# Kernel tuning notes

Measured on AMD Instinct MI355X. Metric: run time of the kernel, lower is better.

Reference implementation:

```python
import jax, jax.numpy as jnp
import numpy as np

N, E, D_IN, HD, H = 50000, 800000, 768, 64, 4
HC = HD * H


def _gat(x, src, dst, etypes, lin_w, att_src, att_dst, edge_emb, lin_edge_w, att_edge,
         bias, res_w, res_b, ln_g, ln_b):
    # Faithful PyG GATConv (edge_dim, concat=True, add_self_loops=True with
    # fill_value='mean', negative_slope=0.2) + residual + LayerNorm. Eval mode: no dropout.
    n = x.shape[0]
    h, c = att_src.shape
    xs = (x @ lin_w).reshape(n, h, c)                      # [N,H,C]
    a_src = jnp.einsum('nhc,hc->nh', xs, att_src)          # [N,H]
    a_dst = jnp.einsum('nhc,hc->nh', xs, att_dst)
    eattr = edge_emb[etypes]                               # [E,ed]
    ones = jnp.ones((etypes.shape[0],), x.dtype)
    cnt = jax.ops.segment_sum(ones, dst, num_segments=n)
    # self-loop edge_attr = mean of incoming edge attrs per node (fill_value='mean')
    loop_attr = jax.ops.segment_sum(eattr, dst, num_segments=n) / jnp.maximum(cnt, 1.0)[:, None]
    loop = jnp.arange(n, dtype=src.dtype)
    src_a = jnp.concatenate([src, loop])
    dst_a = jnp.concatenate([dst, loop])
    e_all = jnp.concatenate([eattr, loop_attr], 0)
    a_edge = jnp.einsum('ehc,hc->eh', (e_all @ lin_edge_w).reshape(-1, h, c), att_edge)
    alpha = jax.nn.leaky_relu(a_src[src_a] + a_dst[dst_a] + a_edge, 0.2)   # [Ea,H]
    # edge softmax over incoming edges of each destination node
    amax = jax.ops.segment_max(alpha, dst_a, num_segments=n)
    ea = jnp.exp(alpha - amax[dst_a])
    denom = jax.ops.segment_sum(ea, dst_a, num_segments=n)
    w = ea / (denom[dst_a] + 1e-16)
    out = jax.ops.segment_sum(xs[src_a] * w[:, :, None], dst_a, num_segments=n)
    out = out.reshape(n, h * c) + bias + (x @ res_w + res_b)
    mu = out.mean(-1, keepdims=True)
    var = jnp.mean((out - mu) ** 2, -1, keepdims=True)
    return (out - mu) * jax.lax.rsqrt(var + 1e-5) * ln_g + ln_b


def _forward(features, positions,
             fe_w1, fe_b1, fe_w2, fe_b2, fe_pos_w, fe_pos_b, fe_type_emb, fe_out_w, fe_out_b,
             g1_lin_w, g1_att_src, g1_att_dst, g1_edge_emb, g1_lin_edge_w, g1_att_edge,
             g1_bias, g1_res_w, g1_res_b, g1_ln_g, g1_ln_b,
             g2_lin_w, g2_att_src, g2_att_dst, g2_edge_emb, g2_lin_edge_w, g2_att_edge,
             g2_bias, g2_res_w, g2_res_b, g2_ln_g, g2_ln_b,
             cls_w, cls_b,
             edge_index, aspect_indices, edge_types, node_types):
    # EnhancedFeatureExtractor (eval: dropout = identity)
    hfe = jax.nn.relu(features @ fe_w1 + fe_b1) @ fe_w2 + fe_b2
    hfe = hfe + fe_type_emb[node_types] + positions[:, None] @ fe_pos_w + fe_pos_b
    hfe = hfe @ fe_out_w + fe_out_b
    src, dst = edge_index[0], edge_index[1]
    hid = _gat(hfe, src, dst, edge_types, g1_lin_w, g1_att_src, g1_att_dst, g1_edge_emb,
               g1_lin_edge_w, g1_att_edge, g1_bias, g1_res_w, g1_res_b, g1_ln_g, g1_ln_b)
    hid = jax.nn.relu(hid)
    hid = _gat(hid, src, dst, edge_types, g2_lin_w, g2_att_src, g2_att_dst, g2_edge_emb,
               g2_lin_edge_w, g2_att_edge, g2_bias, g2_res_w, g2_res_b, g2_ln_g, g2_ln_b)
    return hid[aspect_indices] @ cls_w + cls_b


def setup_inputs() -> dict:
    key = jax.random.key(0)
    ks = jax.random.split(key, 40)
    d = {}
    d['features'] = jax.random.normal(ks[0], (N, D_IN), jnp.float32)
    d['edge_index'] = jax.random.randint(ks[1], (2, E), 0, N, jnp.int32)
    d['aspect_indices'] = jax.random.randint(ks[2], (4096,), 0, N, jnp.int32)
    d['edge_types'] = jax.random.randint(ks[3], (E,), 0, 4, jnp.int32)
    d['node_types'] = jax.random.randint(ks[4], (N,), 0, 3, jnp.int32)
    d['positions'] = jax.random.uniform(ks[5], (N,), jnp.float32)

    def rn(i, shape, s=0.05):
        return s * jax.random.normal(ks[i], shape, jnp.float32)

    d['fe_w1'] = rn(6, (D_IN, HD)); d['fe_b1'] = rn(7, (HD,))
    d['fe_w2'] = rn(8, (HD, HD));   d['fe_b2'] = rn(9, (HD,))
    d['fe_pos_w'] = rn(10, (1, HD)); d['fe_pos_b'] = rn(11, (HD,))
    d['fe_type_emb'] = rn(12, (3, HD))
    d['fe_out_w'] = rn(13, (HD, HD)); d['fe_out_b'] = rn(14, (HD,))
    d['g1_lin_w'] = rn(15, (HD, HC))
    d['g1_att_src'] = rn(16, (H, HD)); d['g1_att_dst'] = rn(17, (H, HD))
    d['g1_edge_emb'] = rn(18, (4, 4)); d['g1_lin_edge_w'] = rn(19, (4, HC))
    d['g1_att_edge'] = rn(20, (H, HD))
    d['g1_bias'] = rn(21, (HC,)); d['g1_res_w'] = rn(22, (HD, HC)); d['g1_res_b'] = rn(23, (HC,))
    d['g1_ln_g'] = jnp.ones((HC,), jnp.float32); d['g1_ln_b'] = jnp.zeros((HC,), jnp.float32)
    d['g2_lin_w'] = rn(24, (HC, HD))
    d['g2_att_src'] = rn(25, (1, HD)); d['g2_att_dst'] = rn(26, (1, HD))
    d['g2_edge_emb'] = rn(27, (4, 4)); d['g2_lin_edge_w'] = rn(28, (4, HD))
    d['g2_att_edge'] = rn(29, (1, HD))
    d['g2_bias'] = rn(30, (HD,)); d['g2_res_w'] = rn(31, (HC, HD)); d['g2_res_b'] = rn(32, (HD,))
    d['g2_ln_g'] = jnp.ones((HD,), jnp.float32); d['g2_ln_b'] = jnp.zeros((HD,), jnp.float32)
    d['cls_w'] = rn(33, (HD, 3)); d['cls_b'] = rn(34, (3,))
    return d


def reference(features, edge_index, aspect_indices, edge_types, node_types, positions,
              fe_w1, fe_b1, fe_w2, fe_b2, fe_pos_w, fe_pos_b, fe_type_emb, fe_out_w, fe_out_b,
              g1_lin_w, g1_att_src, g1_att_dst, g1_edge_emb, g1_lin_edge_w, g1_att_edge,
              g1_bias, g1_res_w, g1_res_b, g1_ln_g, g1_ln_b,
              g2_lin_w, g2_att_src, g2_att_dst, g2_edge_emb, g2_lin_edge_w, g2_att_edge,
              g2_bias, g2_res_w, g2_res_b, g2_ln_g, g2_ln_b,
              cls_w, cls_b):
    return _forward(features, positions,
                    fe_w1, fe_b1, fe_w2, fe_b2, fe_pos_w, fe_pos_b, fe_type_emb, fe_out_w, fe_out_b,
                    g1_lin_w, g1_att_src, g1_att_dst, g1_edge_emb, g1_lin_edge_w, g1_att_edge,
                    g1_bias, g1_res_w, g1_res_b, g1_ln_g, g1_ln_b,
                    g2_lin_w, g2_att_src, g2_att_dst, g2_edge_emb, g2_lin_edge_w, g2_att_edge,
                    g2_bias, g2_res_w, g2_res_b, g2_ln_g, g2_ln_b,
                    cls_w, cls_b,
                    edge_index, aspect_indices, edge_types, node_types)
```

## Files before the change

### kernel.cpp

```cpp
#include <hip/hip_runtime.h>


#define LRELU(x) ((x) > 0.f ? (x) : 0.2f * (x))

typedef __attribute__((ext_vector_type(8))) short short8;
typedef __attribute__((ext_vector_type(4))) float floatx4;

__device__ __forceinline__ unsigned short f2bf(float x) {
    union { float f; unsigned int u; } v; v.f = x;
    unsigned int r = (v.u + 0x7FFFu + ((v.u >> 16) & 1u)) >> 16;
    return (unsigned short)r;
}
__device__ __forceinline__ unsigned int cvtpk(float lo, float hi) {
    unsigned int r;
    asm("v_cvt_pk_bf16_f32 %0, %1, %2" : "=v"(r) : "v"(lo), "v"(hi));
    return r;
}
__device__ __forceinline__ float bflo(unsigned int u) {
    return __uint_as_float(u << 16);
}
__device__ __forceinline__ float bfhi(unsigned int u) {
    return __uint_as_float(u & 0xFFFF0000u);
}
__device__ __forceinline__ float bf1(unsigned short u) {
    return __uint_as_float(((unsigned int)u) << 16);
}

__global__ __launch_bounds__(64) void k_tables(
    const float* __restrict__ e_emb1, const float* __restrict__ lew1,
    const float* __restrict__ ae1,
    const float* __restrict__ e_emb2, const float* __restrict__ lew2,
    const float* __restrict__ ae2,
    float* __restrict__ aet1, float* __restrict__ aet2)
{
    __shared__ float M1[16];
    __shared__ float M2[4];
    int t = threadIdx.x;
    if (t < 16) {
        int d = t >> 2, h = t & 3;
        float s = 0.f;
        for (int c = 0; c < 64; ++c) s += lew1[d * 256 + h * 64 + c] * ae1[h * 64 + c];
        M1[d * 4 + h] = s;
    }
    if (t < 4) {
        float s = 0.f;
        for (int c = 0; c < 64; ++c) s += lew2[t * 64 + c] * ae2[c];
        M2[t] = s;
    }
    __syncthreads();
    if (t < 16) {
        int ty = t >> 2, h = t & 3;
        float s = 0.f;
        for (int d = 0; d < 4; ++d) s += e_emb1[ty * 4 + d] * M1[d * 4 + h];
        aet1[ty * 4 + h] = s;
    }
    if (t < 4) {
        float s = 0.f;
        for (int d = 0; d < 4; ++d) s += e_emb2[t * 4 + d] * M2[d];
        aet2[t] = s;
    }
}

__global__ __launch_bounds__(256) void k_bswz_fe1(
    const float* __restrict__ w1, unsigned short* __restrict__ out)
{
    for (int idx = blockIdx.x * 256 + threadIdx.x; idx < 768 * 64;
         idx += gridDim.x * 256) {
        int k = idx >> 6, col = idx & 63;
        int c = k >> 6, kl = k & 63, kg = kl >> 3, j = kl & 7;
        out[((c * 8 + kg) * 64 + col) * 8 + j] = f2bf(w1[k * 64 + col]);
    }
}

template<int K, int NH>
__global__ __launch_bounds__(256) void k_bswz2(
    const float* __restrict__ B1, const float* __restrict__ B2,
    unsigned short* __restrict__ out)
{
    const int NC = 2 * NH;
    for (int idx = blockIdx.x * 256 + threadIdx.x; idx < K * NC;
         idx += gridDim.x * 256) {
        int k = idx / NC, col = idx % NC;
        float v = (col < NH) ? B1[k * NH + col] : B2[k * NH + col - NH];
        int c = k >> 6, kl = k & 63, kg = kl >> 3, j = kl & 7;
        int ct = col >> 7, cl = col & 127;
        out[(((c * (NC / 128) + ct) * 8 + kg) * 128 + cl) * 8 + j] = f2bf(v);
    }
}

__global__ __launch_bounds__(256) void k_fuse1(
    const float* __restrict__ w2, const float* __restrict__ outw,
    const float* __restrict__ b2, const float* __restrict__ posb,
    const float* __restrict__ outb, const float* __restrict__ temb,
    const float* __restrict__ posw,
    float* __restrict__ W2p, float* __restrict__ h0,
    float* __restrict__ tadd, float* __restrict__ padd)
{
    int t = threadIdx.x;
    int i = t >> 2, jq = (t & 3) * 16;
    float a16[16];
#pragma unroll
    for (int u = 0; u < 16; ++u) a16[u] = 0.f;
    for (int k = 0; k < 64; ++k) {
        float a = w2[i * 64 + k];
        const float* op = outw + k * 64 + jq;
        float4 o0 = *(const float4*)op;
        float4 o1 = *(const float4*)(op + 4);
        float4 o2 = *(const float4*)(op + 8);
        float4 o3 = *(const float4*)(op + 12);
        a16[0] += a * o0.x;  a16[1] += a * o0.y;  a16[2] += a * o0.z;  a16[3] += a * o0.w;
        a16[4] += a * o1.x;  a16[5] += a * o1.y;  a16[6] += a * o1.z;  a16[7] += a * o1.w;
        a16[8] += a * o2.x;  a16[9] += a * o2.y;  a16[10] += a * o2.z; a16[11] += a * o2.w;
        a16[12] += a * o3.x; a16[13] += a * o3.y; a16[14] += a * o3.z; a16[15] += a * o3.w;
    }
#pragma unroll
    for (int u = 0; u < 16; ++u) W2p[i * 64 + jq + u] = a16[u];
    for (int e = t; e < 320; e += 256) {
        int g = e >> 6, j = e & 63;
        float s = 0.f;
        for (int k = 0; k < 64; ++k) {
            float v;
            if (g == 0) v = b2[k] + posb[k];
            else if (g <= 3) v = temb[(g - 1) * 64 + k];
            else v = posw[k];
            s += v * outw[k * 64 + j];
        }
        if (g == 0) h0[j] = s + outb[j];
        else if (g <= 3) tadd[(g - 1) * 64 + j] = s;
        else padd[j] = s;
    }
}

__global__ __launch_bounds__(64) void k_fuse2(
    const float* __restrict__ W2p, const float* __restrict__ h0,
    const float* __restrict__ tadd, const float* __restrict__ padd,
    const float* __restrict__ lin_w, const float* __restrict__ res_w,
    const float* __restrict__ bias, const float* __restrict__ res_b,
    unsigned short* __restrict__ bz, float* __restrict__ C0,
    float* __restrict__ T, float* __restrict__ P)
{
    __shared__ float bcol[64];
    int c = blockIdx.x;
    int j = threadIdx.x;
    int cL = c & 255;
    const float* Bsrc = (c < 256) ? lin_w : res_w;
    float bv = Bsrc[j * 256 + cL];
    bcol[j] = bv;
    __syncthreads();
    float s = 0.f;
#pragma unroll 8
    for (int k = 0; k < 64; ++k) s += W2p[j * 64 + k] * bcol[k];
    int kg = j >> 3, jj = j & 7, ct = c >> 7, cl = c & 127;
    bz[((ct * 8 + kg) * 128 + cl) * 8 + jj] = f2bf(s);
    float pc = h0[j] * bv;
    float p0 = tadd[j] * bv, p1 = tadd[64 + j] * bv, p2 = tadd[128 + j] * bv;
    float pp = padd[j] * bv;
#pragma unroll
    for (int k = 32; k; k >>= 1) {
        pc += __shfl_xor(pc, k, 64); p0 += __shfl_xor(p0, k, 64);
        p1 += __shfl_xor(p1, k, 64); p2 += __shfl_xor(p2, k, 64);
        pp += __shfl_xor(pp, k, 64);
    }
    if (j == 0) {
        C0[c] = pc + ((c >= 256) ? (bias[cL] + res_b[cL]) : 0.f);
        T[c] = p0; T[512 + c] = p1; T[1024 + c] = p2;
        P[c] = pp;
    }
}

__global__ __launch_bounds__(256) void k_fe1(
    const float* __restrict__ feat, const unsigned short* __restrict__ bswz,
    const float* __restrict__ b1, unsigned short* __restrict__ t1b, int N)
{
    __shared__ __align__(16) unsigned short A_lds[8 * 64 * 8];
    int t = threadIdx.x;
    int wv = t >> 6, lane = t & 63;
    int quad = lane >> 4, l16 = lane & 15;
    long n0 = (long)blockIdx.x * 64;

    floatx4 acc[4];
#pragma unroll
    for (int i = 0; i < 4; ++i) acc[i] = (floatx4){0.f, 0.f, 0.f, 0.f};

    int srow = t >> 2, sf4 = t & 3;
    long arow = n0 + srow;
    if (arow >= N) arow = N - 1;
    const float* fbase = feat + arow * 768 + sf4 * 16;
    int col = wv * 16 + l16;

    float4 v0 = *(const float4*)(fbase);
    float4 v1 = *(const float4*)(fbase + 4);
    float4 v2 = *(const float4*)(fbase + 8);
    float4 v3 = *(const float4*)(fbase + 12);

    for (int kc = 0; kc < 768; kc += 64) {
        uint4 w0 = {cvtpk(v0.x, v0.y), cvtpk(v0.z, v0.w),
                    cvtpk(v1.x, v1.y), cvtpk(v1.z, v1.w)};
        uint4 w1p = {cvtpk(v2.x, v2.y), cvtpk(v2.z, v2.w),
                     cvtpk(v3.x, v3.y), cvtpk(v3.z, v3.w)};
        __syncthreads();
        *(uint4*)&A_lds[((2 * sf4) * 64 + srow) * 8] = w0;
        *(uint4*)&A_lds[((2 * sf4 + 1) * 64 + srow) * 8] = w1p;
        if (kc + 64 < 768) {
            v0 = *(const float4*)(fbase + kc + 64);
            v1 = *(const float4*)(fbase + kc + 68);
            v2 = *(const float4*)(fbase + kc + 72);
            v3 = *(const float4*)(fbase + kc + 76);
        }
        __syncthreads();
        int ci = kc >> 6;
#pragma unroll
        for (int s = 0; s < 2; ++s) {
            int kg0 = s * 4 + quad;
            short8 bfrag = *(const short8*)&bswz[((ci * 8 + kg0) * 64 + col) * 8];
#pragma unroll
            for (int mt = 0; mt < 4; ++mt) {
                short8 afrag = *(const short8*)&A_lds[(kg0 * 64 + mt * 16 + l16) * 8];
                acc[mt] = __builtin_amdgcn_mfma_f32_16x16x32_bf16(
                    afrag, bfrag, acc[mt], 0, 0, 0);
            }
        }
    }
    float bb = b1[col];
#pragma unroll
    for (int mt = 0; mt < 4; ++mt) {
#pragma unroll
        for (int r = 0; r < 4; ++r) {
            long m = n0 + mt * 16 + quad * 4 + r;
            if (m < N) t1b[m * 64 + col] = f2bf(fmaxf(acc[mt][r] + bb, 0.f));
        }
    }
}

template<int K, int NH, bool FADD>
__global__ __launch_bounds__(256) void k_prep(
    const unsigned short* __restrict__ A, const unsigned short* __restrict__ bswz,
    const float* __restrict__ c0_or_bias, const float* __restrict__ t_or_resb,
    const float* __restrict__ Ptab, const int* __restrict__ ntypes,
    const float* __restrict__ pos,
    unsigned short* __restrict__ xsb, float* __restrict__ resp, int N)
{
    constexpr int CT = (2 * NH) / 128;
    __shared__ __align__(16) unsigned short A_lds[8 * 64 * 8];
    int t = threadIdx.x;
    int wv = t >> 6, lane = t & 63;
    int quad = lane >> 4, l16 = lane & 15;
    long n0 = (long)blockIdx.x * 64;
    int by = blockIdx.y;

    floatx4 acc[4][2];
#pragma unroll
    for (int i = 0; i < 4; ++i)
#pragma unroll
        for (int j = 0; j < 2; ++j) acc[i][j] = (floatx4){0.f, 0.f, 0.f, 0.f};

    int srow = t >> 2, sf4 = t & 3;
    long arow = n0 + srow;
    if (arow >= N) arow = N - 1;
    const unsigned short* abase = A + arow * (long)K + sf4 * 16;

    uint4 q0 = *(const uint4*)(abase);
    uint4 q1 = *(const uint4*)(abase + 8);

    for (int kc = 0; kc < K; kc += 64) {
        __syncthreads();
        *(uint4*)&A_lds[((2 * sf4) * 64 + srow) * 8] = q0;
        *(uint4*)&A_lds[((2 * sf4 + 1) * 64 + srow) * 8] = q1;
        if (kc + 64 < K) {
            q0 = *(const uint4*)(abase + kc + 64);
            q1 = *(const uint4*)(abase + kc + 64 + 8);
        }
        __syncthreads();
        int ci = kc >> 6;
#pragma unroll
        for (int s = 0; s < 2; ++s) {
            int kg0 = s * 4 + quad;
#pragma unroll
            for (int nt = 0; nt < 2; ++nt) {
                short8 bfrag = *(const short8*)&bswz[
                    (((ci * CT + by) * 8 + kg0) * 128 + wv * 32 + nt * 16 + l16) * 8];
#pragma unroll
                for (int mt = 0; mt < 4; ++mt) {
                    short8 afrag = *(const short8*)&A_lds[(kg0 * 64 + mt * 16 + l16) * 8];
                    acc[mt][nt] = __builtin_amdgcn_mfma_f32_16x16x32_bf16(
                        afrag, bfrag, acc[mt][nt], 0, 0, 0);
                }
            }
        }
    }

    int nta[4][4];
    float posa[4][4];
    if constexpr (FADD) {
#pragma unroll
        for (int mt = 0; mt < 4; ++mt)
#pragma unroll
            for (int r = 0; r < 4; ++r) {
                long m = n0 + mt * 16 + quad * 4 + r;
                if (m < N) { nta[mt][r] = ntypes[m]; posa[mt][r] = pos[m]; }
                else       { nta[mt][r] = 0; posa[mt][r] = 0.f; }
            }
    }
#pragma unroll
    for (int nt = 0; nt < 2; ++nt) {
        int gc = by * 128 + wv * 32 + nt * 16 + l16;
        bool isl = gc < NH;
        int oc = isl ? gc : gc - NH;
        if constexpr (FADD) {
            float c0 = c0_or_bias[gc];
            float pcf = Ptab[gc];
#pragma unroll
            for (int mt = 0; mt < 4; ++mt) {
#pragma unroll
                for (int r = 0; r < 4; ++r) {
                    long m = n0 + mt * 16 + quad * 4 + r;
                    if (m < N) {
                        float val = acc[mt][nt][r] + c0 +
                                    t_or_resb[nta[mt][r] * (2 * NH) + gc] +
                                    posa[mt][r] * pcf;
                        if (isl) xsb[m * NH + oc] = f2bf(val);
                        else     resp[m * NH + oc] = val;
                    }
                }
            }
        } else {
            float badd = isl ? 0.f : (c0_or_bias[oc] + t_or_resb[oc]);
#pragma unroll
            for (int mt = 0; mt < 4; ++mt) {
#pragma unroll
                for (int r = 0; r < 4; ++r) {
                    long m = n0 + mt * 16 + quad * 4 + r;
                    if (m < N) {
                        float val = acc[mt][nt][r];
                        if (isl) xsb[m * NH + oc] = f2bf(val);
                        else     resp[m * NH + oc] = val + badd;
                    }
                }
            }
        }
    }
}

template<int H>
__global__ __launch_bounds__(256) void k_att(
    const unsigned short* __restrict__ xsb, const float* __restrict__ att_s,
    const float* __restrict__ att_d, float* __restrict__ a_src,
    float* __restrict__ a_dst, int N)
{
    int t = threadIdx.x;
    int wv = t >> 6, lane = t & 63;
    long n = (long)blockIdx.x * 4 + wv;
    if (n >= N) return;
    if (H == 4) {
        ushort4 u = *(const ushort4*)&xsb[n * 256 + lane * 4];
        float4 as = *(const float4*)&att_s[lane * 4];
        float4 ad = *(const float4*)&att_d[lane * 4];
        float x0 = bf1(u.x), x1 = bf1(u.y), x2 = bf1(u.z), x3 = bf1(u.w);
        float p = x0 * as.x + x1 * as.y + x2 * as.z + x3 * as.w;
        float q = x0 * ad.x + x1 * ad.y + x2 * ad.z + x3 * ad.w;
#pragma unroll
        for (int k = 8; k; k >>= 1) {
            p += __shfl_xor(p, k, 64);
            q += __shfl_xor(q, k, 64);
        }
        if ((lane & 15) == 0) {
            a_src[n * 4 + (lane >> 4)] = p;
            a_dst[n * 4 + (lane >> 4)] = q;
        }
    } else {
        float x = bf1(xsb[n * 64 + lane]);
        float p = x * att_s[lane];
        float q = x * att_d[lane];
#pragma unroll
        for (int k = 32; k; k >>= 1) {
            p += __shfl_xor(p, k, 64);
            q += __shfl_xor(q, k, 64);
        }
        if (lane == 0) { a_src[n] = p; a_dst[n] = q; }
    }
}

__global__ __launch_bounds__(256) void k_count(
    const int* __restrict__ dst, const int* __restrict__ et,
    int* __restrict__ cnt_t, int E)
{
    int e = blockIdx.x * 256 + threadIdx.x;
    if (e < E) atomicAdd(&cnt_t[dst[e] * 4 + et[e]], 1);
}

__global__ __launch_bounds__(256) void k_scan1(
    const int* __restrict__ cnt_t, int* __restrict__ row_off,
    int* __restrict__ blk_sums, int N)
{
    __shared__ int s[256];
    int t = threadIdx.x;
    int i = blockIdx.x * 256 + t;
    int v = 0;
    if (i < N) v = cnt_t[4 * i] + cnt_t[4 * i + 1] + cnt_t[4 * i + 2] + cnt_t[4 * i + 3];
    s[t] = v;
    __syncthreads();
    for (int off = 1; off < 256; off <<= 1) {
        int x = 0;
        if (t >= off) x = s[t - off];
        __syncthreads();
        s[t] += x;
        __syncthreads();
    }
    if (i < N) row_off[i] = s[t] - v;
    if (t == 255) blk_sums[blockIdx.x] = s[255];
}

__global__ __launch_bounds__(256) void k_scan2(int* __restrict__ blk_sums, int nb)
{
    __shared__ int s[256];
    int t = threadIdx.x;
    int v = (t < nb) ? blk_sums[t] : 0;
    s[t] = v;
    __syncthreads();
    for (int off = 1; off < 256; off <<= 1) {
        int x = 0;
        if (t >= off) x = s[t - off];
        __syncthreads();
        s[t] += x;
        __syncthreads();
    }
    if (t < nb) blk_sums[t] = s[t] - v;
}

__global__ __launch_bounds__(256) void k_scan3(
    int* __restrict__ row_off, int* __restrict__ cursor,
    const int* __restrict__ blk_sums, int N, int E)
{
    int t = threadIdx.x;
    int i = blockIdx.x * 256 + t;
    if (i < N) {
        int o = row_off[i] + blk_sums[blockIdx.x];
        row_off[i] = o;
        cursor[i] = o;
    }
    if (i == 0) row_off[N] = E;
}

__global__ __launch_bounds__(256) void k_scatter(
    const int* __restrict__ src, const int* __restrict__ dst,
    const int* __restrict__ et, int* __restrict__ cursor,
    int* __restrict__ csr_pack, int E)
{
    int e = blockIdx.x * 256 + threadIdx.x;
    if (e < E) {
        int d = dst[e];
        int pos = atomicAdd(&cursor[d], 1);
        csr_pack[pos] = src[e] | (et[e] << 28);
    }
}

__global__ __launch_bounds__(128) void k_gat1(
    const unsigned short* __restrict__ xs1b, const float* __restrict__ a_src,
    const float* __restrict__ a_dst, const int* __restrict__ row_off,
    const int* __restrict__ csr_pack,
    const int* __restrict__ cnt_t, const float* __restrict__ aet1,
    const float* __restrict__ ln_g, const float* __restrict__ ln_b,
    const float* __restrict__ res, unsigned short* __restrict__ out)
{
    __shared__ __align__(16) float4 ws[2][64];
    __shared__ float2 aetp[2][4];
    __shared__ float red[4];
    int n = blockIdx.x;
    int t = threadIdx.x;
    int w = t >> 6, c = t & 63;
    int lc = c & 15, g = c >> 4;
    int h0 = 2 * w;
    if (t < 8) {
        int w2 = t >> 2, ty = t & 3;
        aetp[w2][ty] = make_float2(aet1[ty * 4 + 2 * w2], aet1[ty * 4 + 2 * w2 + 1]);
    }
    int off = row_off[n], deg = row_off[n + 1] - off;
    float2 a_d = *(const float2*)&a_dst[n * 4 + h0];
    __syncthreads();
    float ael0 = 0.f, ael1 = 0.f;
    int degc = 0;
#pragma unroll
    for (int ty = 0; ty < 4; ++ty) {
        int ct = cnt_t[n * 4 + ty];
        degc += ct;
        float2 ae = aetp[w][ty];
        ael0 += (float)ct * ae.x;
        ael1 += (float)ct * ae.y;
    }
    float inv = (degc > 0) ? 1.f / (float)degc : 1.f;
    float2 a_s_self = *(const float2*)&a_src[n * 4 + h0];
    float al0 = a_s_self.x + a_d.x + ael0 * inv;
    float al1 = a_s_self.y + a_d.y + ael1 * inv;
    al0 = LRELU(al0); al1 = LRELU(al1);
    float wself0 = expf(al0), wself1 = expf(al1);

    int col0 = w * 128 + lc * 8;
    const unsigned short* xrow = xs1b + col0;
    float acc[8];
#pragma unroll
    for (int j = 0; j < 8; ++j) acc[j] = 0.f;
    float dp0 = 0.f, dp1 = 0.f;

    for (int base = 0; base < deg; base += 64) {
        int cnt = min(64, deg - base);
        float w0 = 0.f, w1 = 0.f;
        int s = 0;
        if (c < cnt) {
            int pk = csr_pack[off + base + c];
            s = pk & 0x0FFFFFFF;
            int ty = ((unsigned)pk) >> 28;
            float2 as2 = *(const float2*)&a_src[s * 4 + h0];
            float2 ae = aetp[w][ty];
            float a0 = as2.x + a_d.x + ae.x;
            float a1 = as2.y + a_d.y + ae.y;
            a0 = LRELU(a0); a1 = LRELU(a1);
            w0 = expf(a0); w1 = expf(a1);
        }
        dp0 += w0; dp1 += w1;
        ws[w][c] = make_float4(w0, w1, __int_as_float(s), 0.f);
        int cr = (cnt + 7) & ~7;
        for (int i = 0; i < cr; i += 8) {
#pragma unroll
            for (int u = 0; u < 2; ++u) {
                float4 p = ws[w][i + u * 4 + g];
                float wl = (lc < 8) ? p.x : p.y;
                uint4 q = *(const uint4*)&xrow[(long)__float_as_int(p.z) * 256];
                acc[0] += wl * bflo(q.x); acc[1] += wl * bfhi(q.x);
                acc[2] += wl * bflo(q.y); acc[3] += wl * bfhi(q.y);
                acc[4] += wl * bflo(q.z); acc[5] += wl * bfhi(q.z);
                acc[6] += wl * bflo(q.w); acc[7] += wl * bfhi(q.w);
            }
        }
    }
#pragma unroll
    for (int k = 32; k; k >>= 1) {
        dp0 += __shfl_xor(dp0, k, 64);
        dp1 += __shfl_xor(dp1, k, 64);
    }
#pragma unroll
    for (int j = 0; j < 8; ++j) {
        acc[j] += __shfl_xor(acc[j], 16, 64);
        acc[j] += __shfl_xor(acc[j], 32, 64);
    }
    uint4 us = *(const uint4*)&xrow[(long)n * 256];
    float wself_l = (lc < 8) ? wself0 : wself1;
    acc[0] += wself_l * bflo(us.x); acc[1] += wself_l * bfhi(us.x);
    acc[2] += wself_l * bflo(us.y); acc[3] += wself_l * bfhi(us.y);
    acc[4] += wself_l * bflo(us.z); acc[5] += wself_l * bfhi(us.z);
    acc[6] += wself_l * bflo(us.w); acc[7] += wself_l * bfhi(us.w);
    float dsum = ((lc < 8) ? dp0 + wself0 : dp1 + wself1) + 1e-16f;
    float rd = 1.f / dsum;
    float4 r0 = *(const float4*)&res[(long)n * 256 + col0];
    float4 r1 = *(const float4*)&res[(long)n * 256 + col0 + 4];
    float v[8];
    v[0] = acc[0] * rd + r0.x; v[1] = acc[1] * rd + r0.y;
    v[2] = acc[2] * rd + r0.z; v[3] = acc[3] * rd + r0.w;
    v[4] = acc[4] * rd + r1.x; v[5] = acc[5] * rd + r1.y;
    v[6] = acc[6] * rd + r1.z; v[7] = acc[7] * rd + r1.w;
    float s1 = 0.f, s2 = 0.f;
#pragma unroll
    for (int j = 0; j < 8; ++j) { s1 += v[j]; s2 += v[j] * v[j]; }
#pragma unroll
    for (int k = 32; k; k >>= 1) {
        s1 += __shfl_xor(s1, k, 64);
        s2 += __shfl_xor(s2, k, 64);
    }
    if (c == 0) { red[w] = s1 * 0.25f; red[2 + w] = s2 * 0.25f; }
    __syncthreads();
    float mu = (red[0] + red[1]) * (1.f / 256.f);
    float var = (red[2] + red[3]) * (1.f / 256.f) - mu * mu;
    float rs = rsqrtf(var + 1e-5f);
    if (g == 0) {
        float4 lg0 = *(const float4*)&ln_g[col0];
        float4 lg1 = *(const float4*)&ln_g[col0 + 4];
        float4 lb0 = *(const float4*)&ln_b[col0];
        float4 lb1 = *(const float4*)&ln_b[col0 + 4];
        float y[8];
        y[0] = fmaxf((v[0] - mu) * rs * lg0.x + lb0.x, 0.f);
        y[1] = fmaxf((v[1] - mu) * rs * lg0.y + lb0.y, 0.f);
        y[2] = fmaxf((v[2] - mu) * rs * lg0.z + lb0.z, 0.f);
        y[3] = fmaxf((v[3] - mu) * rs * lg0.w + lb0.w, 0.f);
        y[4] = fmaxf((v[4] - mu) * rs * lg1.x + lb1.x, 0.f);
        y[5] = fmaxf((v[5] - mu) * rs * lg1.y + lb1.y, 0.f);
        y[6] = fmaxf((v[6] - mu) * rs * lg1.z + lb1.z, 0.f);
        y[7] = fmaxf((v[7] - mu) * rs * lg1.w + lb1.w, 0.f);
        uint4 o;
        o.x = cvtpk(y[0], y[1]); o.y = cvtpk(y[2], y[3]);
        o.z = cvtpk(y[4], y[5]); o.w = cvtpk(y[6], y[7]);
        *(uint4*)&out[(long)n * 256 + col0] = o;
    }
}

__global__ __launch_bounds__(64) void k_gat2(
    const unsigned short* __restrict__ xs2b, const float* __restrict__ a_src,
    const float* __restrict__ a_dst, const int* __restrict__ row_off,
    const int* __restrict__ csr_pack,
    const int* __restrict__ cnt_t, const float* __restrict__ aet2,
    const float* __restrict__ ln_g, const float* __restrict__ ln_b,
    float* io)
{
    __shared__ __align__(8) float2 ws[64];
    __shared__ float aetl[4];
    int n = blockIdx.x;
    int c = threadIdx.x;
    int lc = c & 15, g = c >> 4;
    if (c < 4) aetl[c] = aet2[c];
    int off = row_off[n], deg = row_off[n + 1] - off;
    float a_d = a_dst[n];
    float ael = 0.f;
    int degc = 0;
#pragma unroll
    for (int ty = 0; ty < 4; ++ty) {
        int ct = cnt_t[n * 4 + ty];
        degc += ct;
        ael += (float)ct * aet2[ty];
    }
    ael *= (degc > 0 ? 1.f / (float)degc : 1.f);
    float al = a_src[n] + a_d + ael;
    al = LRELU(al);
    float wself = expf(al);

    int colb = lc * 4;
    const unsigned short* xrow = xs2b + colb;
    float acc[4] = {0.f, 0.f, 0.f, 0.f};
    float dp = 0.f;
    for (int base = 0; base < deg; base += 64) {
        int cnt = min(64, deg - base);
        float we = 0.f;
        int s = 0;
        if (c < cnt) {
            int pk = csr_pack[off + base + c];
            s = pk & 0x0FFFFFFF;
            int ty = ((unsigned)pk) >> 28;
            float a = a_src[s] + a_d + aetl[ty];
            a = LRELU(a);
            we = expf(a);
        }
        dp += we;
        ws[c] = make_float2(we, __int_as_float(s));
        int cr = (cnt + 7) & ~7;
        for (int i = 0; i < cr; i += 8) {
#pragma unroll
            for (int u = 0; u < 2; ++u) {
                float2 p = ws[i + u * 4 + g];
                uint2 q = *(const uint2*)&xrow[(long)__float_as_int(p.y) * 64];
                acc[0] += p.x * bflo(q.x); acc[1] += p.x * bfhi(q.x);
                acc[2] += p.x * bflo(q.y); acc[3] += p.x * bfhi(q.y);
            }
        }
    }
#pragma unroll
    for (int k = 32; k; k >>= 1) dp += __shfl_xor(dp, k, 64);
#pragma unroll
    for (int j = 0; j < 4; ++j) {
        acc[j] += __shfl_xor(acc[j], 16, 64);
        acc[j] += __shfl_xor(acc[j], 32, 64);
    }
    uint2 us = *(const uint2*)&xrow[(long)n * 64];
    acc[0] += wself * bflo(us.x); acc[1] += wself * bfhi(us.x);
    acc[2] += wself * bflo(us.y); acc[3] += wself * bfhi(us.y);
    float dsum = dp + wself + 1e-16f;
    float rd = 1.f / dsum;
    float4 r = *(const float4*)&io[(long)n * 64 + colb];
    float v[4];
    v[0] = acc[0] * rd + r.x; v[1] = acc[1] * rd + r.y;
    v[2] = acc[2] * rd + r.z; v[3] = acc[3] * rd + r.w;
    float s1 = v[0] + v[1] + v[2] + v[3];
    float s2 = v[0] * v[0] + v[1] * v[1] + v[2] * v[2] + v[3] * v[3];
#pragma unroll
    for (int k = 32; k; k >>= 1) {
        s1 += __shfl_xor(s1, k, 64);
        s2 += __shfl_xor(s2, k, 64);
    }
    float mu = s1 * (1.f / 256.f);
    float var = s2 * (1.f / 256.f) - mu * mu;
    float rs = rsqrtf(var + 1e-5f);
    if (g == 0) {
        float4 lg = *(const float4*)&ln_g[colb];
        float4 lb = *(const float4*)&ln_b[colb];
        float4 y;
        y.x = (v[0] - mu) * rs * lg.x + lb.x;
        y.y = (v[1] - mu) * rs * lg.y + lb.y;
        y.z = (v[2] - mu) * rs * lg.z + lb.z;
        y.w = (v[3] - mu) * rs * lg.w + lb.w;
        *(float4*)&io[(long)n * 64 + colb] = y;
    }
}

__global__ __launch_bounds__(256) void k_cls(
    const float* __restrict__ hid2, const int* __restrict__ asp,
    const float* __restrict__ w, const float* __restrict__ b,
    float* __restrict__ out)
{
    int g = blockIdx.x * 256 + threadIdx.x;
    int i = g / 3, j = g - i * 3;
    int a = asp[i];
    float acc = b[j];
#pragma unroll 8
    for (int cc = 0; cc < 64; ++cc) acc += hid2[(long)a * 64 + cc] * w[cc * 3 + j];
    out[i * 3 + j] = acc;
}

extern "C" void kernel_launch(void* const* d_in, const int* in_sizes, int n_in,
                              void* d_out, int out_size, void* d_ws, size_t ws_size,
                              hipStream_t stream)
{
    const float* features    = (const float*)d_in[0];
    const int*   edge_index  = (const int*)d_in[1];
    const int*   aspect      = (const int*)d_in[2];
    const int*   etypes      = (const int*)d_in[3];
    const int*   ntypes      = (const int*)d_in[4];
    const float* pos         = (const float*)d_in[5];
    const float* fe_w1       = (const float*)d_in[6];
    const float* fe_b1       = (const float*)d_in[7];
    const float* fe_w2       = (const float*)d_in[8];
    const float* fe_b2       = (const float*)d_in[9];
    const float* fe_pos_w    = (const float*)d_in[10];
    const float* fe_pos_b    = (const float*)d_in[11];
    const float* fe_type_emb = (const float*)d_in[12];
    const float* fe_out_w    = (const float*)d_in[13];
    const float* fe_out_b    = (const float*)d_in[14];
    const float* g1_lin_w    = (const float*)d_in[15];
    const float* g1_att_src  = (const float*)d_in[16];
    const float* g1_att_dst  = (const float*)d_in[17];
    const float* g1_edge_emb = (const float*)d_in[18];
    const float* g1_lin_edge = (const float*)d_in[19];
    const float* g1_att_edge = (const float*)d_in[20];
    const float* g1_bias     = (const float*)d_in[21];
    const float* g1_res_w    = (const float*)d_in[22];
    const float* g1_res_b    = (const float*)d_in[23];
    const float* g1_ln_g     = (const float*)d_in[24];
    const float* g1_ln_b     = (const float*)d_in[25];
    const float* g2_lin_w    = (const float*)d_in[26];
    const float* g2_att_src  = (const float*)d_in[27];
    const float* g2_att_dst  = (const float*)d_in[28];
    const float* g2_edge_emb = (const float*)d_in[29];
    const float* g2_lin_edge = (const float*)d_in[30];
    const float* g2_att_edge = (const float*)d_in[31];
    const float* g2_bias     = (const float*)d_in[32];
    const float* g2_res_w    = (const float*)d_in[33];
    const float* g2_res_b    = (const float*)d_in[34];
    const float* g2_ln_g     = (const float*)d_in[35];
    const float* g2_ln_b     = (const float*)d_in[36];
    const float* cls_w       = (const float*)d_in[37];
    const float* cls_b       = (const float*)d_in[38];

    const int N = in_sizes[0] / 768;
    const int E = in_sizes[1] / 2;
    const int* src = edge_index;
    const int* dst = edge_index + E;

    char* wsb = (char*)d_ws;
    size_t off = 0;
    auto alloc = [&](size_t bytes) -> char* {
        char* p = wsb + off;
        off += (bytes + 255) & ~(size_t)255;
        return p;
    };
    unsigned short* t1b  = (unsigned short*)alloc((size_t)N * 64 * 2);
    unsigned short* xs1b = (unsigned short*)alloc((size_t)N * 256 * 2);
    unsigned short* xs2b = (unsigned short*)alloc((size_t)N * 64 * 2);
    unsigned short* hid1b= (unsigned short*)alloc((size_t)N * 256 * 2);
    float* rp1     = (float*)alloc((size_t)N * 256 * 4);
    float* rp2     = (float*)alloc((size_t)N * 64 * 4);
    float* a_src1  = (float*)alloc((size_t)N * 4 * 4);
    float* a_dst1  = (float*)alloc((size_t)N * 4 * 4);
    float* a_src2  = (float*)alloc((size_t)N * 4);
    float* a_dst2  = (float*)alloc((size_t)N * 4);
    int*   cnt_t   = (int*)alloc((size_t)N * 4 * 4);
    int*   row_off = (int*)alloc((size_t)(N + 1) * 4);
    int*   cursor  = (int*)alloc((size_t)N * 4);
    int*   blk     = (int*)alloc(1024);
    int*   csr_pack= (int*)alloc((size_t)E * 4);
    float* aet1    = (float*)alloc(64);
    float* aet2    = (float*)alloc(64);
    unsigned short* bz_fe1 = (unsigned short*)alloc(768 * 64 * 2);
    unsigned short* bz_p1  = (unsigned short*)alloc(64 * 512 * 2);
    unsigned short* bz_p2  = (unsigned short*)alloc(256 * 128 * 2);
    float* W2p     = (float*)alloc(64 * 64 * 4);
    float* h0v     = (float*)alloc(64 * 4);
    float* taddv   = (float*)alloc(192 * 4);
    float* paddv   = (float*)alloc(64 * 4);
    float* C0t     = (float*)alloc(512 * 4);
    float* Tt      = (float*)alloc(3 * 512 * 4);
    float* Pt      = (float*)alloc(512 * 4);

    hipMemsetAsync(cnt_t, 0, (size_t)N * 4 * 4, stream);

    int mb = (N + 63) / 64;
    int ab = (N + 3) / 4;

    k_tables<<<1, 64, 0, stream>>>(g1_edge_emb, g1_lin_edge, g1_att_edge,
                                   g2_edge_emb, g2_lin_edge, g2_att_edge, aet1, aet2);
    k_bswz_fe1<<<48, 256, 0, stream>>>(fe_w1, bz_fe1);
    k_fuse1<<<1, 256, 0, stream>>>(fe_w2, fe_out_w, fe_b2, fe_pos_b, fe_out_b,
                                   fe_type_emb, fe_pos_w, W2p, h0v, taddv, paddv);
    k_fuse2<<<512, 64, 0, stream>>>(W2p, h0v, taddv, paddv, g1_lin_w, g1_res_w,
                                    g1_bias, g1_res_b, bz_p1, C0t, Tt, Pt);
    k_bswz2<256, 64><<<32, 256, 0, stream>>>(g2_lin_w, g2_res_w, bz_p2);
    k_fe1<<<mb, 256, 0, stream>>>(features, bz_fe1, fe_b1, t1b, N);
    k_prep<64, 256, true><<<dim3(mb, 4), 256, 0, stream>>>(
        t1b, bz_p1, C0t, Tt, Pt, ntypes, pos, xs1b, rp1, N);
    k_att<4><<<ab, 256, 0, stream>>>(xs1b, g1_att_src, g1_att_dst, a_src1, a_dst1, N);
    int eblk = (E + 255) / 256;
    int nb = (N + 255) / 256;
    k_count<<<eblk, 256, 0, stream>>>(dst, etypes, cnt_t, E);
    k_scan1<<<nb, 256, 0, stream>>>(cnt_t, row_off, blk, N);
    k_scan2<<<1, 256, 0, stream>>>(blk, nb);
    k_scan3<<<nb, 256, 0, stream>>>(row_off, cursor, blk, N, E);
    k_scatter<<<eblk, 256, 0, stream>>>(src, dst, etypes, cursor, csr_pack, E);
    k_gat1<<<N, 128, 0, stream>>>(xs1b, a_src1, a_dst1, row_off, csr_pack,
                                  cnt_t, aet1, g1_ln_g, g1_ln_b, rp1, hid1b);
    k_prep<256, 64, false><<<dim3(mb, 1), 256, 0, stream>>>(
        hid1b, bz_p2, g2_bias, g2_res_b, nullptr, nullptr, nullptr, xs2b, rp2, N);
    k_att<1><<<ab, 256, 0, stream>>>(xs2b, g2_att_src, g2_att_dst, a_src2, a_dst2, N);
    k_gat2<<<N, 64, 0, stream>>>(xs2b, a_src2, a_dst2, row_off, csr_pack,
                                 cnt_t, aet2, g2_ln_g, g2_ln_b, rp2);
    k_cls<<<(out_size + 255) / 256, 256, 0, stream>>>(rp2, aspect, cls_w, cls_b,
                                                      (float*)d_out);
}
```

Before: 641.4 us.

## Merge setup kernels, drop LDS staging in GEMMs, store layer-1 residual as bf16

```diff
diff --git a/kernel.cpp b/kernel.cpp
--- a/kernel.cpp
+++ b/kernel.cpp
@@ -26,69 +26,12 @@
     return __uint_as_float(((unsigned int)u) << 16);
 }
 
-__global__ __launch_bounds__(64) void k_tables(
+__global__ __launch_bounds__(256) void k_pre0(
     const float* __restrict__ e_emb1, const float* __restrict__ lew1,
     const float* __restrict__ ae1,
     const float* __restrict__ e_emb2, const float* __restrict__ lew2,
     const float* __restrict__ ae2,
-    float* __restrict__ aet1, float* __restrict__ aet2)
-{
-    __shared__ float M1[16];
-    __shared__ float M2[4];
-    int t = threadIdx.x;
-    if (t < 16) {
-        int d = t >> 2, h = t & 3;
-        float s = 0.f;
-        for (int c = 0; c < 64; ++c) s += lew1[d * 256 + h * 64 + c] * ae1[h * 64 + c];
-        M1[d * 4 + h] = s;
-    }
-    if (t < 4) {
-        float s = 0.f;
-        for (int c = 0; c < 64; ++c) s += lew2[t * 64 + c] * ae2[c];
-        M2[t] = s;
-    }
-    __syncthreads();
-    if (t < 16) {
-        int ty = t >> 2, h = t & 3;
-        float s = 0.f;
-        for (int d = 0; d < 4; ++d) s += e_emb1[ty * 4 + d] * M1[d * 4 + h];
-        aet1[ty * 4 + h] = s;
-    }
-    if (t < 4) {
-        float s = 0.f;
-        for (int d = 0; d < 4; ++d) s += e_emb2[t * 4 + d] * M2[d];
-        aet2[t] = s;
-    }
-}
-
-__global__ __launch_bounds__(256) void k_bswz_fe1(
-    const float* __restrict__ w1, unsigned short* __restrict__ out)
-{
-    for (int idx = blockIdx.x * 256 + threadIdx.x; idx < 768 * 64;
-         idx += gridDim.x * 256) {
-        int k = idx >> 6, col = idx & 63;
-        int c = k >> 6, kl = k & 63, kg = kl >> 3, j = kl & 7;
-        out[((c * 8 + kg) * 64 + col) * 8 + j] = f2bf(w1[k * 64 + col]);
-    }
-}
-
-template<int K, int NH>
-__global__ __launch_bounds__(256) void k_bswz2(
-    const float* __restrict__ B1, const float* __restrict__ B2,
-    unsigned short* __restrict__ out)
-{
-    const int NC = 2 * NH;
-    for (int idx = blockIdx.x * 256 + threadIdx.x; idx < K * NC;
-         idx += gridDim.x * 256) {
-        int k = idx / NC, col = idx % NC;
-        float v = (col < NH) ? B1[k * NH + col] : B2[k * NH + col - NH];
-        int c = k >> 6, kl = k & 63, kg = kl >> 3, j = kl & 7;
-        int ct = col >> 7, cl = col & 127;
-        out[(((c * (NC / 128) + ct) * 8 + kg) * 128 + cl) * 8 + j] = f2bf(v);
-    }
-}
-
-__global__ __launch_bounds__(256) void k_fuse1(
+    float* __restrict__ aet1, float* __restrict__ aet2,
     const float* __restrict__ w2, const float* __restrict__ outw,
     const float* __restrict__ b2, const float* __restrict__ posb,
     const float* __restrict__ outb, const float* __restrict__ temb,
@@ -96,38 +39,85 @@
     float* __restrict__ W2p, float* __restrict__ h0,
     float* __restrict__ tadd, float* __restrict__ padd)
 {
-    int t = threadIdx.x;
-    int i = t >> 2, jq = (t & 3) * 16;
-    float a16[16];
-#pragma unroll
-    for (int u = 0; u < 16; ++u) a16[u] = 0.f;
-    for (int k = 0; k < 64; ++k) {
-        float a = w2[i * 64 + k];
-        const float* op = outw + k * 64 + jq;
-        float4 o0 = *(const float4*)op;
-        float4 o1 = *(const float4*)(op + 4);
-        float4 o2 = *(const float4*)(op + 8);
-        float4 o3 = *(const float4*)(op + 12);
-        a16[0] += a * o0.x;  a16[1] += a * o0.y;  a16[2] += a * o0.z;  a16[3] += a * o0.w;
-        a16[4] += a * o1.x;  a16[5] += a * o1.y;  a16[6] += a * o1.z;  a16[7] += a * o1.w;
-        a16[8] += a * o2.x;  a16[9] += a * o2.y;  a16[10] += a * o2.z; a16[11] += a * o2.w;
-        a16[12] += a * o3.x; a16[13] += a * o3.y; a16[14] += a * o3.z; a16[15] += a * o3.w;
-    }
-#pragma unroll
-    for (int u = 0; u < 16; ++u) W2p[i * 64 + jq + u] = a16[u];
-    for (int e = t; e < 320; e += 256) {
-        int g = e >> 6, j = e & 63;
-        float s = 0.f;
+    __shared__ float M1[16];
+    __shared__ float M2[4];
+    int t = threadIdx.x;
+    if (blockIdx.x == 0) {
+        if (t < 16) {
+            int d = t >> 2, h = t & 3;
+            float s = 0.f;
+            for (int c = 0; c < 64; ++c) s += lew1[d * 256 + h * 64 + c] * ae1[h * 64 + c];
+            M1[d * 4 + h] = s;
+        }
+        if (t < 4) {
+            float s = 0.f;
+            for (int c = 0; c < 64; ++c) s += lew2[t * 64 + c] * ae2[c];
+            M2[t] = s;
+        }
+        __syncthreads();
+        if (t < 16) {
+            int ty = t >> 2, h = t & 3;
+            float s = 0.f;
+            for (int d = 0; d < 4; ++d) s += e_emb1[ty * 4 + d] * M1[d * 4 + h];
+            aet1[ty * 4 + h] = s;
+        }
+        if (t < 4) {
+            float s = 0.f;
+            for (int d = 0; d < 4; ++d) s += e_emb2[t * 4 + d] * M2[d];
+            aet2[t] = s;
+        }
+    } else {
+        int i = t >> 2, jq = (t & 3) * 16;
+        float a16[16];
+#pragma unroll
+        for (int u = 0; u < 16; ++u) a16[u] = 0.f;
         for (int k = 0; k < 64; ++k) {
-            float v;
-            if (g == 0) v = b2[k] + posb[k];
-            else if (g <= 3) v = temb[(g - 1) * 64 + k];
-            else v = posw[k];
-            s += v * outw[k * 64 + j];
-        }
-        if (g == 0) h0[j] = s + outb[j];
-        else if (g <= 3) tadd[(g - 1) * 64 + j] = s;
-        else padd[j] = s;
+            float a = w2[i * 64 + k];
+            const float* op = outw + k * 64 + jq;
+            float4 o0 = *(const float4*)op;
+            float4 o1 = *(const float4*)(op + 4);
+            float4 o2 = *(const float4*)(op + 8);
+            float4 o3 = *(const float4*)(op + 12);
+            a16[0] += a * o0.x;  a16[1] += a * o0.y;  a16[2] += a * o0.z;  a16[3] += a * o0.w;
+            a16[4] += a * o1.x;  a16[5] += a * o1.y;  a16[6] += a * o1.z;  a16[7] += a * o1.w;
+            a16[8] += a * o2.x;  a16[9] += a * o2.y;  a16[10] += a * o2.z; a16[11] += a * o2.w;
+            a16[12] += a * o3.x; a16[13] += a * o3.y; a16[14] += a * o3.z; a16[15] += a * o3.w;
+        }
+#pragma unroll
+        for (int u = 0; u < 16; ++u) W2p[i * 64 + jq + u] = a16[u];
+        for (int e = t; e < 320; e += 256) {
+            int g = e >> 6, j = e & 63;
+            float s = 0.f;
+            for (int k = 0; k < 64; ++k) {
+                float v;
+                if (g == 0) v = b2[k] + posb[k];
+                else if (g <= 3) v = temb[(g - 1) * 64 + k];
+                else v = posw[k];
+                s += v * outw[k * 64 + j];
+            }
+            if (g == 0) h0[j] = s + outb[j];
+            else if (g <= 3) tadd[(g - 1) * 64 + j] = s;
+            else padd[j] = s;
+        }
+    }
+}
+
+__global__ __launch_bounds__(256) void k_bswz(
+    const float* __restrict__ w1, const float* __restrict__ B1,
+    const float* __restrict__ B2,
+    unsigned short* __restrict__ out_fe1, unsigned short* __restrict__ out_p2)
+{
+    int idx = blockIdx.x * 256 + threadIdx.x;
+    if (idx < 768 * 64) {
+        int k = idx >> 6, col = idx & 63;
+        int c = k >> 6, kl = k & 63, kg = kl >> 3, j = kl & 7;
+        out_fe1[((c * 8 + kg) * 64 + col) * 8 + j] = f2bf(w1[k * 64 + col]);
+    } else {
+        int i2 = idx - 768 * 64;
+        int k = i2 >> 7, col = i2 & 127;
+        float v = (col < 64) ? B1[k * 64 + col] : B2[k * 64 + col - 64];
+        int c = k >> 6, kl = k & 63, kg = kl >> 3, j = kl & 7;
+        out_p2[((c * 8 + kg) * 128 + col) * 8 + j] = f2bf(v);
     }
 }
 
@@ -172,170 +162,158 @@
     const float* __restrict__ feat, const unsigned short* __restrict__ bswz,
     const float* __restrict__ b1, unsigned short* __restrict__ t1b, int N)
 {
-    __shared__ __align__(16) unsigned short A_lds[8 * 64 * 8];
     int t = threadIdx.x;
     int wv = t >> 6, lane = t & 63;
     int quad = lane >> 4, l16 = lane & 15;
-    long n0 = (long)blockIdx.x * 64;
+    long rw = (long)blockIdx.x * 64 + wv * 16;
+    long ra = rw + l16;
+    if (ra >= N) ra = N - 1;
+    const float* fbase = feat + ra * 768 + quad * 8;
 
     floatx4 acc[4];
 #pragma unroll
     for (int i = 0; i < 4; ++i) acc[i] = (floatx4){0.f, 0.f, 0.f, 0.f};
 
-    int srow = t >> 2, sf4 = t & 3;
-    long arow = n0 + srow;
-    if (arow >= N) arow = N - 1;
-    const float* fbase = feat + arow * 768 + sf4 * 16;
-    int col = wv * 16 + l16;
-
-    float4 v0 = *(const float4*)(fbase);
-    float4 v1 = *(const float4*)(fbase + 4);
-    float4 v2 = *(const float4*)(fbase + 8);
-    float4 v3 = *(const float4*)(fbase + 12);
-
-    for (int kc = 0; kc < 768; kc += 64) {
-        uint4 w0 = {cvtpk(v0.x, v0.y), cvtpk(v0.z, v0.w),
-                    cvtpk(v1.x, v1.y), cvtpk(v1.z, v1.w)};
-        uint4 w1p = {cvtpk(v2.x, v2.y), cvtpk(v2.z, v2.w),
-                     cvtpk(v3.x, v3.y), cvtpk(v3.z, v3.w)};
-        __syncthreads();
-        *(uint4*)&A_lds[((2 * sf4) * 64 + srow) * 8] = w0;
-        *(uint4*)&A_lds[((2 * sf4 + 1) * 64 + srow) * 8] = w1p;
-        if (kc + 64 < 768) {
-            v0 = *(const float4*)(fbase + kc + 64);
-            v1 = *(const float4*)(fbase + kc + 68);
-            v2 = *(const float4*)(fbase + kc + 72);
-            v3 = *(const float4*)(fbase + kc + 76);
-        }
-        __syncthreads();
-        int ci = kc >> 6;
+    for (int ci = 0; ci < 12; ++ci) {
+        const float* fc = fbase + ci * 64;
+        short8 af[2];
 #pragma unroll
         for (int s = 0; s < 2; ++s) {
-            int kg0 = s * 4 + quad;
-            short8 bfrag = *(const short8*)&bswz[((ci * 8 + kg0) * 64 + col) * 8];
-#pragma unroll
-            for (int mt = 0; mt < 4; ++mt) {
-                short8 afrag = *(const short8*)&A_lds[(kg0 * 64 + mt * 16 + l16) * 8];
-                acc[mt] = __builtin_amdgcn_mfma_f32_16x16x32_bf16(
-                    afrag, bfrag, acc[mt], 0, 0, 0);
+            float4 x = *(const float4*)(fc + s * 32);
+            float4 y = *(const float4*)(fc + s * 32 + 4);
+            uint4 u = {cvtpk(x.x, x.y), cvtpk(x.z, x.w),
+                       cvtpk(y.x, y.y), cvtpk(y.z, y.w)};
+            af[s] = *(short8*)&u;
+        }
+#pragma unroll
+        for (int s = 0; s < 2; ++s) {
+            int kg = s * 4 + quad;
+#pragma unroll
+            for (int ct = 0; ct < 4; ++ct) {
+                short8 bfrag = *(const short8*)&bswz[
+                    ((ci * 8 + kg) * 64 + ct * 16 + l16) * 8];
+                acc[ct] = __builtin_amdgcn_mfma_f32_16x16x32_bf16(
+                    af[s], bfrag, acc[ct], 0, 0, 0);
             }
         }
     }
-    float bb = b1[col];
-#pragma unroll
-    for (int mt = 0; mt < 4; ++mt) {
+#pragma unroll
+    for (int ct = 0; ct < 4; ++ct) {
+        float bb = b1[ct * 16 + l16];
 #pragma unroll
         for (int r = 0; r < 4; ++r) {
-            long m = n0 + mt * 16 + quad * 4 + r;
-            if (m < N) t1b[m * 64 + col] = f2bf(fmaxf(acc[mt][r] + bb, 0.f));
-        }
-    }
-}
-
-template<int K, int NH, bool FADD>
-__global__ __launch_bounds__(256) void k_prep(
+            long m = rw + quad * 4 + r;
+            if (m < N)
+                t1b[m * 64 + ct * 16 + l16] = f2bf(fmaxf(acc[ct][r] + bb, 0.f));
+        }
+    }
+}
+
+__global__ __launch_bounds__(256) void k_prep1(
     const unsigned short* __restrict__ A, const unsigned short* __restrict__ bswz,
-    const float* __restrict__ c0_or_bias, const float* __restrict__ t_or_resb,
-    const float* __restrict__ Ptab, const int* __restrict__ ntypes,
+    const float* __restrict__ C0, const float* __restrict__ T,
+    const float* __restrict__ P, const int* __restrict__ ntypes,
     const float* __restrict__ pos,
-    unsigned short* __restrict__ xsb, float* __restrict__ resp, int N)
-{
-    constexpr int CT = (2 * NH) / 128;
-    __shared__ __align__(16) unsigned short A_lds[8 * 64 * 8];
+    unsigned short* __restrict__ xsb, unsigned short* __restrict__ resp, int N)
+{
     int t = threadIdx.x;
     int wv = t >> 6, lane = t & 63;
     int quad = lane >> 4, l16 = lane & 15;
-    long n0 = (long)blockIdx.x * 64;
+    long rw = (long)blockIdx.x * 64 + wv * 16;
     int by = blockIdx.y;
-
-    floatx4 acc[4][2];
-#pragma unroll
-    for (int i = 0; i < 4; ++i)
-#pragma unroll
-        for (int j = 0; j < 2; ++j) acc[i][j] = (floatx4){0.f, 0.f, 0.f, 0.f};
-
-    int srow = t >> 2, sf4 = t & 3;
-    long arow = n0 + srow;
-    if (arow >= N) arow = N - 1;
-    const unsigned short* abase = A + arow * (long)K + sf4 * 16;
-
-    uint4 q0 = *(const uint4*)(abase);
-    uint4 q1 = *(const uint4*)(abase + 8);
-
-    for (int kc = 0; kc < K; kc += 64) {
-        __syncthreads();
-        *(uint4*)&A_lds[((2 * sf4) * 64 + srow) * 8] = q0;
-        *(uint4*)&A_lds[((2 * sf4 + 1) * 64 + srow) * 8] = q1;
-        if (kc + 64 < K) {
-            q0 = *(const uint4*)(abase + kc + 64);
-            q1 = *(const uint4*)(abase + kc + 64 + 8);
-        }
-        __syncthreads();
-        int ci = kc >> 6;
+    long ra = rw + l16;
+    if (ra >= N) ra = N - 1;
+    const unsigned short* abase = A + ra * 64 + quad * 8;
+
+    floatx4 acc[8];
+#pragma unroll
+    for (int i = 0; i < 8; ++i) acc[i] = (floatx4){0.f, 0.f, 0.f, 0.f};
+
+    short8 af[2];
+    af[0] = *(const short8*)(abase);
+    af[1] = *(const short8*)(abase + 32);
+#pragma unroll
+    for (int s = 0; s < 2; ++s) {
+        int kg = s * 4 + quad;
+#pragma unroll
+        for (int c8 = 0; c8 < 8; ++c8) {
+            short8 bfrag = *(const short8*)&bswz[
+                ((by * 8 + kg) * 128 + c8 * 16 + l16) * 8];
+            acc[c8] = __builtin_amdgcn_mfma_f32_16x16x32_bf16(
+                af[s], bfrag, acc[c8], 0, 0, 0);
+        }
+    }
+    int nta[4];
+    float posa[4];
+#pragma unroll
+    for (int r = 0; r < 4; ++r) {
+        long m = rw + quad * 4 + r;
+        if (m < N) { nta[r] = ntypes[m]; posa[r] = pos[m]; }
+        else       { nta[r] = 0; posa[r] = 0.f; }
+    }
+    bool isl = (by < 2);
+    int cb = by * 128;
+#pragma unroll
+    for (int c8 = 0; c8 < 8; ++c8) {
+        int gc = cb + c8 * 16 + l16;
+        float c0 = C0[gc], pcf = P[gc];
+#pragma unroll
+        for (int r = 0; r < 4; ++r) {
+            long m = rw + quad * 4 + r;
+            if (m < N) {
+                float val = acc[c8][r] + c0 + T[nta[r] * 512 + gc] + posa[r] * pcf;
+                if (isl) xsb[m * 256 + gc] = f2bf(val);
+                else     resp[m * 256 + gc - 256] = f2bf(val);
+            }
+        }
+    }
+}
+
+__global__ __launch_bounds__(256) void k_prep2(
+    const unsigned short* __restrict__ A, const unsigned short* __restrict__ bswz,
+    const float* __restrict__ bias, const float* __restrict__ res_b,
+    unsigned short* __restrict__ xsb, float* __restrict__ resp, int N)
+{
+    int t = threadIdx.x;
+    int wv = t >> 6, lane = t & 63;
+    int quad = lane >> 4, l16 = lane & 15;
+    long rw = (long)blockIdx.x * 64 + wv * 16;
+    long ra = rw + l16;
+    if (ra >= N) ra = N - 1;
+    const unsigned short* abase = A + ra * 256 + quad * 8;
+
+    floatx4 acc[8];
+#pragma unroll
+    for (int i = 0; i < 8; ++i) acc[i] = (floatx4){0.f, 0.f, 0.f, 0.f};
+
+    for (int ci = 0; ci < 4; ++ci) {
+        short8 af[2];
+        af[0] = *(const short8*)(abase + ci * 64);
+        af[1] = *(const short8*)(abase + ci * 64 + 32);
 #pragma unroll
         for (int s = 0; s < 2; ++s) {
-            int kg0 = s * 4 + quad;
-#pragma unroll
-            for (int nt = 0; nt < 2; ++nt) {
+            int kg = s * 4 + quad;
+#pragma unroll
+            for (int c8 = 0; c8 < 8; ++c8) {
                 short8 bfrag = *(const short8*)&bswz[
-                    (((ci * CT + by) * 8 + kg0) * 128 + wv * 32 + nt * 16 + l16) * 8];
-#pragma unroll
-                for (int mt = 0; mt < 4; ++mt) {
-                    short8 afrag = *(const short8*)&A_lds[(kg0 * 64 + mt * 16 + l16) * 8];
-                    acc[mt][nt] = __builtin_amdgcn_mfma_f32_16x16x32_bf16(
-                        afrag, bfrag, acc[mt][nt], 0, 0, 0);
-                }
+                    ((ci * 8 + kg) * 128 + c8 * 16 + l16) * 8];
+                acc[c8] = __builtin_amdgcn_mfma_f32_16x16x32_bf16(
+                    af[s], bfrag, acc[c8], 0, 0, 0);
             }
         }
     }
-
-    int nta[4][4];
-    float posa[4][4];
-    if constexpr (FADD) {
-#pragma unroll
-        for (int mt = 0; mt < 4; ++mt)
-#pragma unroll
-            for (int r = 0; r < 4; ++r) {
-                long m = n0 + mt * 16 + quad * 4 + r;
-                if (m < N) { nta[mt][r] = ntypes[m]; posa[mt][r] = pos[m]; }
-                else       { nta[mt][r] = 0; posa[mt][r] = 0.f; }
-            }
-    }
-#pragma unroll
-    for (int nt = 0; nt < 2; ++nt) {
-        int gc = by * 128 + wv * 32 + nt * 16 + l16;
-        bool isl = gc < NH;
-        int oc = isl ? gc : gc - NH;
-        if constexpr (FADD) {
-            float c0 = c0_or_bias[gc];
-            float pcf = Ptab[gc];
-#pragma unroll
-            for (int mt = 0; mt < 4; ++mt) {
-#pragma unroll
-                for (int r = 0; r < 4; ++r) {
-                    long m = n0 + mt * 16 + quad * 4 + r;
-                    if (m < N) {
-                        float val = acc[mt][nt][r] + c0 +
-                                    t_or_resb[nta[mt][r] * (2 * NH) + gc] +
-                                    posa[mt][r] * pcf;
-                        if (isl) xsb[m * NH + oc] = f2bf(val);
-                        else     resp[m * NH + oc] = val;
-                    }
-                }
-            }
-        } else {
-            float badd = isl ? 0.f : (c0_or_bias[oc] + t_or_resb[oc]);
-#pragma unroll
-            for (int mt = 0; mt < 4; ++mt) {
-#pragma unroll
-                for (int r = 0; r < 4; ++r) {
-                    long m = n0 + mt * 16 + quad * 4 + r;
-                    if (m < N) {
-                        float val = acc[mt][nt][r];
-                        if (isl) xsb[m * NH + oc] = f2bf(val);
-                        else     resp[m * NH + oc] = val + badd;
-                    }
-                }
+#pragma unroll
+    for (int c8 = 0; c8 < 8; ++c8) {
+        int gc = c8 * 16 + l16;
+        bool isl = gc < 64;
+        float badd = isl ? 0.f : (bias[gc - 64] + res_b[gc - 64]);
+#pragma unroll
+        for (int r = 0; r < 4; ++r) {
+            long m = rw + quad * 4 + r;
+            if (m < N) {
+                float val = acc[c8][r];
+                if (isl) xsb[m * 64 + gc] = f2bf(val);
+                else     resp[m * 64 + gc - 64] = val + badd;
             }
         }
     }
@@ -460,7 +438,7 @@
     const int* __restrict__ csr_pack,
     const int* __restrict__ cnt_t, const float* __restrict__ aet1,
     const float* __restrict__ ln_g, const float* __restrict__ ln_b,
-    const float* __restrict__ res, unsigned short* __restrict__ out)
+    const unsigned short* __restrict__ res, unsigned short* __restrict__ out)
 {
     __shared__ __align__(16) float4 ws[2][64];
     __shared__ float2 aetp[2][4];
@@ -550,13 +528,12 @@
     acc[6] += wself_l * bflo(us.w); acc[7] += wself_l * bfhi(us.w);
     float dsum = ((lc < 8) ? dp0 + wself0 : dp1 + wself1) + 1e-16f;
     float rd = 1.f / dsum;
-    float4 r0 = *(const float4*)&res[(long)n * 256 + col0];
-    float4 r1 = *(const float4*)&res[(long)n * 256 + col0 + 4];
+    uint4 ur = *(const uint4*)&res[(long)n * 256 + col0];
     float v[8];
-    v[0] = acc[0] * rd + r0.x; v[1] = acc[1] * rd + r0.y;
-    v[2] = acc[2] * rd + r0.z; v[3] = acc[3] * rd + r0.w;
-    v[4] = acc[4] * rd + r1.x; v[5] = acc[5] * rd + r1.y;
-    v[6] = acc[6] * rd + r1.z; v[7] = acc[7] * rd + r1.w;
+    v[0] = acc[0] * rd + bflo(ur.x); v[1] = acc[1] * rd + bfhi(ur.x);
+    v[2] = acc[2] * rd + bflo(ur.y); v[3] = acc[3] * rd + bfhi(ur.y);
+    v[4] = acc[4] * rd + bflo(ur.z); v[5] = acc[5] * rd + bfhi(ur.z);
+    v[6] = acc[6] * rd + bflo(ur.w); v[7] = acc[7] * rd + bfhi(ur.w);
     float s1 = 0.f, s2 = 0.f;
 #pragma unroll
     for (int j = 0; j < 8; ++j) { s1 += v[j]; s2 += v[j] * v[j]; }
@@ -761,7 +738,7 @@
     unsigned short* xs1b = (unsigned short*)alloc((size_t)N * 256 * 2);
     unsigned short* xs2b = (unsigned short*)alloc((size_t)N * 64 * 2);
     unsigned short* hid1b= (unsigned short*)alloc((size_t)N * 256 * 2);
-    float* rp1     = (float*)alloc((size_t)N * 256 * 4);
+    unsigned short* rp1  = (unsigned short*)alloc((size_t)N * 256 * 2);
     float* rp2     = (float*)alloc((size_t)N * 64 * 4);
     float* a_src1  = (float*)alloc((size_t)N * 4 * 4);
     float* a_dst1  = (float*)alloc((size_t)N * 4 * 4);
@@ -790,16 +767,15 @@
     int mb = (N + 63) / 64;
     int ab = (N + 3) / 4;
 
-    k_tables<<<1, 64, 0, stream>>>(g1_edge_emb, g1_lin_edge, g1_att_edge,
-                                   g2_edge_emb, g2_lin_edge, g2_att_edge, aet1, aet2);
-    k_bswz_fe1<<<48, 256, 0, stream>>>(fe_w1, bz_fe1);
-    k_fuse1<<<1, 256, 0, stream>>>(fe_w2, fe_out_w, fe_b2, fe_pos_b, fe_out_b,
-                                   fe_type_emb, fe_pos_w, W2p, h0v, taddv, paddv);
+    k_pre0<<<2, 256, 0, stream>>>(g1_edge_emb, g1_lin_edge, g1_att_edge,
+                                  g2_edge_emb, g2_lin_edge, g2_att_edge, aet1, aet2,
+                                  fe_w2, fe_out_w, fe_b2, fe_pos_b, fe_out_b,
+                                  fe_type_emb, fe_pos_w, W2p, h0v, taddv, paddv);
+    k_bswz<<<320, 256, 0, stream>>>(fe_w1, g2_lin_w, g2_res_w, bz_fe1, bz_p2);
     k_fuse2<<<512, 64, 0, stream>>>(W2p, h0v, taddv, paddv, g1_lin_w, g1_res_w,
                                     g1_bias, g1_res_b, bz_p1, C0t, Tt, Pt);
-    k_bswz2<256, 64><<<32, 256, 0, stream>>>(g2_lin_w, g2_res_w, bz_p2);
     k_fe1<<<mb, 256, 0, stream>>>(features, bz_fe1, fe_b1, t1b, N);
-    k_prep<64, 256, true><<<dim3(mb, 4), 256, 0, stream>>>(
+    k_prep1<<<dim3(mb, 4), 256, 0, stream>>>(
         t1b, bz_p1, C0t, Tt, Pt, ntypes, pos, xs1b, rp1, N);
     k_att<4><<<ab, 256, 0, stream>>>(xs1b, g1_att_src, g1_att_dst, a_src1, a_dst1, N);
     int eblk = (E + 255) / 256;
@@ -811,8 +787,7 @@
     k_scatter<<<eblk, 256, 0, stream>>>(src, dst, etypes, cursor, csr_pack, E);
     k_gat1<<<N, 128, 0, stream>>>(xs1b, a_src1, a_dst1, row_off, csr_pack,
                                   cnt_t, aet1, g1_ln_g, g1_ln_b, rp1, hid1b);
-    k_prep<256, 64, false><<<dim3(mb, 1), 256, 0, stream>>>(
-        hid1b, bz_p2, g2_bias, g2_res_b, nullptr, nullptr, nullptr, xs2b, rp2, N);
+    k_prep2<<<mb, 256, 0, stream>>>(hid1b, bz_p2, g2_bias, g2_res_b, xs2b, rp2, N);
     k_att<1><<<ab, 256, 0, stream>>>(xs2b, g2_att_src, g2_att_dst, a_src2, a_dst2, N);
     k_gat2<<<N, 64, 0, stream>>>(xs2b, a_src2, a_dst2, row_off, csr_pack,
                                  cnt_t, aet2, g2_ln_g, g2_ln_b, rp2);
```

Result: faster. 620.9 us (-3.2%).
